# Performance work log

Hardware: AMD Instinct MI355X
Metric: run time of the kernel (lower is better)

The kernel has to match this reference:

```python
import jax, jax.numpy as jnp
import numpy as np

N, L = 5, 2097152
WIDTH = 11  # max_pool1d kernel width in the original


def setup_inputs() -> dict:
    key = jax.random.key(0)
    k1, k2 = jax.random.split(key)
    rppg = jax.random.normal(k1, (N, L), dtype=jnp.float32)
    ppg = jax.random.normal(k2, (N, L), dtype=jnp.float32)
    return {"rppg": rppg, "ppg": ppg, "fs": 30, "epoch": 15}


def _normalize(x):
    # normalize_torch: per-signal standardization
    mu = x.mean(axis=1, keepdims=True)
    sd = x.std(axis=1, keepdims=True)
    return (x - mu) / sd


def _window_max(x, width):
    # sliding max over centered window of `width`, same padding (-inf pad)
    return jax.lax.reduce_window(x, -jnp.inf, jax.lax.max,
                                 (1, width), (1, 1),
                                 [(0, 0), (width // 2, width // 2)])


def _mean_hr(x, fs):
    # A position p is a 'nice peak' iff max_pool argmax at p equals p,
    # i.e. x[p] is the max of its own centered window (ties have measure 0
    # for continuous signals). unique()+masking collapses to this mask.
    w = _window_max(x, WIDTH)
    m1 = x == w                                            # [N, L] peak mask
    npk = m1.sum(axis=1, keepdims=True).astype(x.dtype)
    mean_pk = (x * m1).sum(axis=1, keepdims=True) / npk    # mean of peak values
    m = m1 & (x > mean_pk / 2)                             # amplitude-filtered peaks
    idx = jnp.arange(x.shape[1])
    vals = jnp.where(m, idx, -1)
    # previous peak index strictly before p (fixed-shape replacement for diff
    # over a variable-length peak index list)
    prev = jnp.pad(jax.lax.cummax(vals, axis=1)[:, :-1], ((0, 0), (1, 0)),
                   constant_values=-1)
    valid = m & (prev >= 0)                                # one entry per inter-peak gap
    gaps = (idx[None, :] - prev).astype(x.dtype)
    inv = jnp.where(valid, 1.0 / gaps, 0.0)
    # mean(60 / (gap / fs)) = 60 * fs * mean(1 / gap)
    return (60.0 * fs) * inv.sum(axis=1) / valid.sum(axis=1).astype(x.dtype)


def reference(rppg, ppg, fs, epoch):
    ppg = _normalize(ppg.reshape(N, -1))
    rppg = _normalize(rppg.reshape(N, -1))
    ppg_hr = _mean_hr(ppg, fs)
    rppg_hr = _mean_hr(rppg, fs)
    # hr_score = mean_i |ppg_hr - rppg_hr| / ppg_hr  (peak_score is computed
    # in the original but not returned)
    return jnp.mean(jnp.abs(ppg_hr - rppg_hr) / ppg_hr)
```

## Files before the change

kernel.cpp:

```cpp
#include <hip/hip_runtime.h>
#include <math.h>
#include <limits.h>

namespace {

constexpr int LNUM = 2097152;
constexpr int NROW = 5;
constexpr int NSER = 10;
constexpr int TPB = 256;
constexpr int CHUNK = 4096;
constexpr int CPR = LNUM / CHUNK;
constexpr int NBLK = NSER * CPR;
constexpr int KIT = 4;

struct Agg { int first; int last; int c; double s; };

__device__ __forceinline__ Agg combine(const Agg& a, const Agg& b) {
  Agg r;
  r.first = (a.first >= 0) ? a.first : b.first;
  r.last  = (b.last >= 0) ? b.last : a.last;
  r.s = a.s + b.s;
  r.c = a.c + b.c;
  if (a.last >= 0 && b.first >= 0) {
    r.s += 1.0 / (double)(b.first - a.last);
    r.c += 1;
  }
  return r;
}

__device__ __forceinline__ const float* row_ptr(const float* rppg,
                                                const float* ppg, int rw) {
  return (rw < NROW) ? rppg + (size_t)rw * LNUM
                     : ppg + (size_t)(rw - NROW) * LNUM;
}

__device__ __forceinline__ void window4(const float* __restrict__ x, int p0,
                                        float X[4], float w[4]) {
  const float4 f = *reinterpret_cast<const float4*>(x + p0);
  X[0] = f.x; X[1] = f.y; X[2] = f.z; X[3] = f.w;
  float Y[14];
  Y[5] = X[0]; Y[6] = X[1]; Y[7] = X[2]; Y[8] = X[3];
  Y[1] = __shfl_up(X[0], 1);  Y[2] = __shfl_up(X[1], 1);
  Y[3] = __shfl_up(X[2], 1);  Y[4] = __shfl_up(X[3], 1);
  Y[0] = __shfl_up(X[3], 2);
  Y[9] = __shfl_down(X[0], 1);  Y[10] = __shfl_down(X[1], 1);
  Y[11] = __shfl_down(X[2], 1); Y[12] = __shfl_down(X[3], 1);
  Y[13] = __shfl_down(X[0], 2);
  const int lane = threadIdx.x & 63;
  if (lane == 0) {
#pragma unroll
    for (int j = 0; j < 5; ++j) {
      int g = p0 - 5 + j;
      Y[j] = (g >= 0) ? x[g] : -INFINITY;
    }
  } else if (lane == 1) {
    int g = p0 - 5;
    Y[0] = (g >= 0) ? x[g] : -INFINITY;
  }
  if (lane == 63) {
#pragma unroll
    for (int j = 0; j < 5; ++j) {
      int g = p0 + 4 + j;
      Y[9 + j] = (g < LNUM) ? x[g] : -INFINITY;
    }
  } else if (lane == 62) {
    int g = p0 + 8;
    Y[13] = (g < LNUM) ? x[g] : -INFINITY;
  }
  float m2[13];
#pragma unroll
  for (int i = 0; i < 13; ++i) m2[i] = fmaxf(Y[i], Y[i + 1]);
  float m4[11];
#pragma unroll
  for (int i = 0; i < 11; ++i) m4[i] = fmaxf(m2[i], m2[i + 2]);
  float m8[7];
#pragma unroll
  for (int i = 0; i < 7; ++i) m8[i] = fmaxf(m4[i], m4[i + 4]);
#pragma unroll
  for (int t = 0; t < 4; ++t) w[t] = fmaxf(m8[t], m8[t + 3]);
}

__global__ __launch_bounds__(TPB) void stats_kernel(
    const float* __restrict__ rppg, const float* __restrict__ ppg,
    double* __restrict__ psum, double* __restrict__ ppk,
    int* __restrict__ pnpk) {
  const int bid = blockIdx.x;
  const int rw = bid >> 9;
  const int chunk = bid & (CPR - 1);
  const float* x = row_ptr(rppg, ppg, rw);
  const int lane = threadIdx.x & 63;
  const int wid = threadIdx.x >> 6;
  const int segbase = chunk * CHUNK + wid * 1024;

  double tsum = 0.0, tpk = 0.0;
  int tn = 0;
  for (int k = 0; k < KIT; ++k) {
    const int p0 = segbase + k * 256 + 4 * lane;
    float X[4], w[4];
    window4(x, p0, X, w);
#pragma unroll
    for (int t = 0; t < 4; ++t) {
      tsum += (double)X[t];
      if (X[t] == w[t]) { tpk += (double)X[t]; ++tn; }
    }
  }
#pragma unroll
  for (int off = 32; off > 0; off >>= 1) {
    tsum += __shfl_down(tsum, off);
    tpk  += __shfl_down(tpk, off);
    tn   += __shfl_down(tn, off);
  }
  __shared__ double wsum[4], wpk[4];
  __shared__ int wn[4];
  if (lane == 0) { wsum[wid] = tsum; wpk[wid] = tpk; wn[wid] = tn; }
  __syncthreads();
  if (threadIdx.x == 0) {
    psum[bid] = wsum[0] + wsum[1] + wsum[2] + wsum[3];
    ppk[bid]  = wpk[0] + wpk[1] + wpk[2] + wpk[3];
    pnpk[bid] = wn[0] + wn[1] + wn[2] + wn[3];
  }
}

__global__ __launch_bounds__(TPB) void thresh_kernel(
    const double* __restrict__ psum, const double* __restrict__ ppk,
    const int* __restrict__ pnpk, double* __restrict__ thr) {
  const int r = blockIdx.x;
  const int t = threadIdx.x;
  const int lane = t & 63;
  const int wid = t >> 6;
  double s0 = psum[r * CPR + t] + psum[r * CPR + t + 256];
  double p0 = ppk[r * CPR + t] + ppk[r * CPR + t + 256];
  int n0 = pnpk[r * CPR + t] + pnpk[r * CPR + t + 256];
#pragma unroll
  for (int off = 32; off > 0; off >>= 1) {
    s0 += __shfl_down(s0, off);
    p0 += __shfl_down(p0, off);
    n0 += __shfl_down(n0, off);
  }
  __shared__ double ws[4], wp[4];
  __shared__ int wn[4];
  if (lane == 0) { ws[wid] = s0; wp[wid] = p0; wn[wid] = n0; }
  __syncthreads();
  if (t == 0) {
    double S = ws[0] + ws[1] + ws[2] + ws[3];
    double P = wp[0] + wp[1] + wp[2] + wp[3];
    double Nn = (double)(wn[0] + wn[1] + wn[2] + wn[3]);
    thr[r] = 0.5 * (S / (double)LNUM + P / Nn);
  }
}

__global__ __launch_bounds__(TPB) void gap_kernel(
    const float* __restrict__ rppg, const float* __restrict__ ppg,
    const double* __restrict__ thr,
    int* __restrict__ cfirst, int* __restrict__ clast,
    double* __restrict__ csum, int* __restrict__ ccnt) {
  const int bid = blockIdx.x;
  const int rw = bid >> 9;
  const int chunk = bid & (CPR - 1);
  const float* x = row_ptr(rppg, ppg, rw);
  const float th = (float)thr[rw];
  const int lane = threadIdx.x & 63;
  const int wid = threadIdx.x >> 6;
  const int segbase = chunk * CHUNK + wid * 1024;

  double lsum = 0.0;
  int lcnt = 0;
  int lfirst = INT_MAX;
  int carry = -1;
  for (int k = 0; k < KIT; ++k) {
    const int p0 = segbase + k * 256 + 4 * lane;
    float X[4], w[4];
    window4(x, p0, X, w);
    int pk = -1;
#pragma unroll
    for (int t = 0; t < 4; ++t)
      if (X[t] == w[t] && X[t] > th) pk = p0 + t;
    if (pk >= 0 && lfirst == INT_MAX) lfirst = pk;
    int m = pk;
#pragma unroll
    for (int off = 1; off < 64; off <<= 1) {
      int u = __shfl_up(m, off);
      if (lane >= off) m = max(m, u);
    }
    int excl = __shfl_up(m, 1);
    int prev = (lane == 0) ? carry : max(excl, carry);
    if (pk >= 0 && prev >= 0) {
      lsum += (double)(1.0f / (float)(pk - prev));
      ++lcnt;
    }
    int lastall = __shfl(m, 63);
    carry = max(carry, lastall);
  }
#pragma unroll
  for (int off = 32; off > 0; off >>= 1) {
    lsum += __shfl_down(lsum, off);
    lcnt += __shfl_down(lcnt, off);
    lfirst = min(lfirst, __shfl_down(lfirst, off));
  }
  __shared__ Agg waggs[4];
  if (lane == 0) {
    Agg a;
    a.first = (lfirst == INT_MAX) ? -1 : lfirst;
    a.last = carry;
    a.c = lcnt; a.s = lsum;
    waggs[wid] = a;
  }
  __syncthreads();
  if (threadIdx.x == 0) {
    Agg r = waggs[0];
    r = combine(r, waggs[1]);
    r = combine(r, waggs[2]);
    r = combine(r, waggs[3]);
    cfirst[bid] = r.first; clast[bid] = r.last;
    csum[bid] = r.s; ccnt[bid] = r.c;
  }
}

__global__ __launch_bounds__(TPB) void final_kernel(
    const int* __restrict__ cfirst, const int* __restrict__ clast,
    const double* __restrict__ csum, const int* __restrict__ ccnt,
    const int* __restrict__ fsp, float* __restrict__ out) {
  __shared__ Agg waggs[4];
  __shared__ double shr[NSER];
  const int t = threadIdx.x;
  const int lane = t & 63;
  const int wid = t >> 6;
  for (int r = 0; r < NSER; ++r) {
    const int i0 = r * CPR + 2 * t;
    Agg a0; a0.first = cfirst[i0];     a0.last = clast[i0];
    a0.c = ccnt[i0];                   a0.s = csum[i0];
    Agg a1; a1.first = cfirst[i0 + 1]; a1.last = clast[i0 + 1];
    a1.c = ccnt[i0 + 1];               a1.s = csum[i0 + 1];
    a0 = combine(a0, a1);
#pragma unroll
    for (int off = 1; off < 64; off <<= 1) {
      Agg b;
      b.first = __shfl_down(a0.first, off);
      b.last  = __shfl_down(a0.last, off);
      b.c     = __shfl_down(a0.c, off);
      b.s     = __shfl_down(a0.s, off);
      a0 = combine(a0, b);
    }
    if (lane == 0) waggs[wid] = a0;
    __syncthreads();
    if (t == 0) {
      Agg rr = waggs[0];
      rr = combine(rr, waggs[1]);
      rr = combine(rr, waggs[2]);
      rr = combine(rr, waggs[3]);
      shr[r] = 60.0 * (double)fsp[0] * rr.s / (double)rr.c;
    }
    __syncthreads();
  }
  if (t == 0) {
    double acc = 0.0;
    for (int r = 0; r < NROW; ++r)
      acc += fabs(shr[NROW + r] - shr[r]) / shr[NROW + r];
    out[0] = (float)(acc / (double)NROW);
  }
}

}

extern "C" void kernel_launch(void* const* d_in, const int* in_sizes, int n_in,
                              void* d_out, int out_size, void* d_ws, size_t ws_size,
                              hipStream_t stream) {
  const float* rppg = (const float*)d_in[0];
  const float* ppg  = (const float*)d_in[1];
  const int* fsp    = (const int*)d_in[2];
  float* out        = (float*)d_out;
  char* ws          = (char*)d_ws;

  double* psum   = (double*)(ws);
  double* ppk    = (double*)(ws + 40960);
  int*    pnpk   = (int*)(ws + 81920);
  double* csum   = (double*)(ws + 102400);
  int*    cfirst = (int*)(ws + 143360);
  int*    clast  = (int*)(ws + 163840);
  int*    ccnt   = (int*)(ws + 184320);
  double* thr    = (double*)(ws + 204800);

  stats_kernel<<<NBLK, TPB, 0, stream>>>(rppg, ppg, psum, ppk, pnpk);
  thresh_kernel<<<NSER, TPB, 0, stream>>>(psum, ppk, pnpk, thr);
  gap_kernel<<<NBLK, TPB, 0, stream>>>(rppg, ppg, thr, cfirst, clast, csum, ccnt);
  final_kernel<<<1, TPB, 0, stream>>>(cfirst, clast, csum, ccnt, fsp, out);
  (void)in_sizes; (void)n_in; (void)out_size; (void)ws_size;
}
```

Baseline: 170.7 us.

## Compact peak candidates in first pass so gap pass avoids rereading signals

The stats pass now writes each wavefront's local-max candidates (position and value) into compacted per-region slots using ballot and popcount. The gap pass reads only these compacted candidates and applies the threshold, instead of rereading the full 80 MB of input and recomputing window maxima. Final reduction now combines four times as many per-wavefront aggregates, and combine uses float reciprocal to match per-gap precision. Risk: the fixed slot size of 172 per 1024-element region assumes a bounded peak count, and extra scattered writes add traffic to the first pass.

```diff
diff --git a/kernel.cpp b/kernel.cpp
--- a/kernel.cpp
+++ b/kernel.cpp
@@ -12,6 +12,9 @@
 constexpr int CPR = LNUM / CHUNK;
 constexpr int NBLK = NSER * CPR;
 constexpr int KIT = 4;
+constexpr int SLOT = 172;
+constexpr int NREG = NBLK * 4;
+constexpr int RPR = NREG / NSER;
 
 struct Agg { int first; int last; int c; double s; };
 
@@ -22,7 +25,7 @@
   r.s = a.s + b.s;
   r.c = a.c + b.c;
   if (a.last >= 0 && b.first >= 0) {
-    r.s += 1.0 / (double)(b.first - a.last);
+    r.s += (double)(1.0f / (float)(b.first - a.last));
     r.c += 1;
   }
   return r;
@@ -83,7 +86,9 @@
 __global__ __launch_bounds__(TPB) void stats_kernel(
     const float* __restrict__ rppg, const float* __restrict__ ppg,
     double* __restrict__ psum, double* __restrict__ ppk,
-    int* __restrict__ pnpk) {
+    int* __restrict__ pnpk,
+    int* __restrict__ wpos, float* __restrict__ wval,
+    int* __restrict__ wcnt) {
   const int bid = blockIdx.x;
   const int rw = bid >> 9;
   const int chunk = bid & (CPR - 1);
@@ -91,19 +96,34 @@
   const int lane = threadIdx.x & 63;
   const int wid = threadIdx.x >> 6;
   const int segbase = chunk * CHUNK + wid * 1024;
+  const int region = bid * 4 + wid;
+  const int wbase = region * SLOT;
 
   double tsum = 0.0, tpk = 0.0;
   int tn = 0;
+  int wcount = 0;
   for (int k = 0; k < KIT; ++k) {
     const int p0 = segbase + k * 256 + 4 * lane;
     float X[4], w[4];
     window4(x, p0, X, w);
+    int off = -1;
+    float pv = 0.0f;
 #pragma unroll
     for (int t = 0; t < 4; ++t) {
       tsum += (double)X[t];
-      if (X[t] == w[t]) { tpk += (double)X[t]; ++tn; }
-    }
-  }
+      if (X[t] == w[t]) { tpk += (double)X[t]; ++tn; off = t; pv = X[t]; }
+    }
+    const bool cand = (off >= 0);
+    const unsigned long long bal = __ballot(cand);
+    const int rank = __popcll(bal & ((1ull << lane) - 1ull));
+    if (cand) {
+      wpos[wbase + wcount + rank] = p0 + off;
+      wval[wbase + wcount + rank] = pv;
+    }
+    wcount += __popcll(bal);
+  }
+  if (lane == 0) wcnt[region] = wcount;
+
 #pragma unroll
   for (int off = 32; off > 0; off >>= 1) {
     tsum += __shfl_down(tsum, off);
@@ -149,32 +169,30 @@
   }
 }
 
-__global__ __launch_bounds__(TPB) void gap_kernel(
-    const float* __restrict__ rppg, const float* __restrict__ ppg,
-    const double* __restrict__ thr,
-    int* __restrict__ cfirst, int* __restrict__ clast,
-    double* __restrict__ csum, int* __restrict__ ccnt) {
-  const int bid = blockIdx.x;
-  const int rw = bid >> 9;
-  const int chunk = bid & (CPR - 1);
-  const float* x = row_ptr(rppg, ppg, rw);
-  const float th = (float)thr[rw];
+__global__ __launch_bounds__(TPB) void gapc_kernel(
+    const int* __restrict__ wpos, const float* __restrict__ wval,
+    const int* __restrict__ wcnt, const double* __restrict__ thr,
+    int* __restrict__ afirst, int* __restrict__ alast,
+    double* __restrict__ asum, int* __restrict__ acnt) {
   const int lane = threadIdx.x & 63;
   const int wid = threadIdx.x >> 6;
-  const int segbase = chunk * CHUNK + wid * 1024;
+  const int region = blockIdx.x * 4 + wid;
+  const int rw = region / RPR;
+  const float th = (float)thr[rw];
+  const int cnt = wcnt[region];
+  const int base = region * SLOT;
 
   double lsum = 0.0;
   int lcnt = 0;
   int lfirst = INT_MAX;
   int carry = -1;
-  for (int k = 0; k < KIT; ++k) {
-    const int p0 = segbase + k * 256 + 4 * lane;
-    float X[4], w[4];
-    window4(x, p0, X, w);
+  for (int k = 0; k < 3; ++k) {
+    const int i = k * 64 + lane;
     int pk = -1;
-#pragma unroll
-    for (int t = 0; t < 4; ++t)
-      if (X[t] == w[t] && X[t] > th) pk = p0 + t;
+    if (i < cnt) {
+      float v = wval[base + i];
+      if (v > th) pk = wpos[base + i];
+    }
     if (pk >= 0 && lfirst == INT_MAX) lfirst = pk;
     int m = pk;
 #pragma unroll
@@ -197,28 +215,17 @@
     lcnt += __shfl_down(lcnt, off);
     lfirst = min(lfirst, __shfl_down(lfirst, off));
   }
-  __shared__ Agg waggs[4];
   if (lane == 0) {
-    Agg a;
-    a.first = (lfirst == INT_MAX) ? -1 : lfirst;
-    a.last = carry;
-    a.c = lcnt; a.s = lsum;
-    waggs[wid] = a;
-  }
-  __syncthreads();
-  if (threadIdx.x == 0) {
-    Agg r = waggs[0];
-    r = combine(r, waggs[1]);
-    r = combine(r, waggs[2]);
-    r = combine(r, waggs[3]);
-    cfirst[bid] = r.first; clast[bid] = r.last;
-    csum[bid] = r.s; ccnt[bid] = r.c;
+    afirst[region] = (lfirst == INT_MAX) ? -1 : lfirst;
+    alast[region] = carry;
+    acnt[region] = lcnt;
+    asum[region] = lsum;
   }
 }
 
 __global__ __launch_bounds__(TPB) void final_kernel(
-    const int* __restrict__ cfirst, const int* __restrict__ clast,
-    const double* __restrict__ csum, const int* __restrict__ ccnt,
+    const int* __restrict__ afirst, const int* __restrict__ alast,
+    const double* __restrict__ asum, const int* __restrict__ acnt,
     const int* __restrict__ fsp, float* __restrict__ out) {
   __shared__ Agg waggs[4];
   __shared__ double shr[NSER];
@@ -226,12 +233,15 @@
   const int lane = t & 63;
   const int wid = t >> 6;
   for (int r = 0; r < NSER; ++r) {
-    const int i0 = r * CPR + 2 * t;
-    Agg a0; a0.first = cfirst[i0];     a0.last = clast[i0];
-    a0.c = ccnt[i0];                   a0.s = csum[i0];
-    Agg a1; a1.first = cfirst[i0 + 1]; a1.last = clast[i0 + 1];
-    a1.c = ccnt[i0 + 1];               a1.s = csum[i0 + 1];
-    a0 = combine(a0, a1);
+    const int i0 = r * RPR + 8 * t;
+    Agg a0; a0.first = afirst[i0]; a0.last = alast[i0];
+    a0.c = acnt[i0];               a0.s = asum[i0];
+#pragma unroll
+    for (int j = 1; j < 8; ++j) {
+      Agg aj; aj.first = afirst[i0 + j]; aj.last = alast[i0 + j];
+      aj.c = acnt[i0 + j];               aj.s = asum[i0 + j];
+      a0 = combine(a0, aj);
+    }
 #pragma unroll
     for (int off = 1; off < 64; off <<= 1) {
       Agg b;
@@ -274,15 +284,20 @@
   double* psum   = (double*)(ws);
   double* ppk    = (double*)(ws + 40960);
   int*    pnpk   = (int*)(ws + 81920);
-  double* csum   = (double*)(ws + 102400);
-  int*    cfirst = (int*)(ws + 143360);
-  int*    clast  = (int*)(ws + 163840);
-  int*    ccnt   = (int*)(ws + 184320);
-  double* thr    = (double*)(ws + 204800);
-
-  stats_kernel<<<NBLK, TPB, 0, stream>>>(rppg, ppg, psum, ppk, pnpk);
+  double* thr    = (double*)(ws + 102400);
+  int*    afirst = (int*)(ws + 103424);
+  int*    alast  = (int*)(ws + 185344);
+  int*    acnt   = (int*)(ws + 267264);
+  double* asum   = (double*)(ws + 349184);
+  int*    wcnt   = (int*)(ws + 513024);
+  int*    wpos   = (int*)(ws + 594944);
+  float*  wval   = (float*)(ws + 14685184);
+
+  stats_kernel<<<NBLK, TPB, 0, stream>>>(rppg, ppg, psum, ppk, pnpk,
+                                         wpos, wval, wcnt);
   thresh_kernel<<<NSER, TPB, 0, stream>>>(psum, ppk, pnpk, thr);
-  gap_kernel<<<NBLK, TPB, 0, stream>>>(rppg, ppg, thr, cfirst, clast, csum, ccnt);
-  final_kernel<<<1, TPB, 0, stream>>>(cfirst, clast, csum, ccnt, fsp, out);
+  gapc_kernel<<<NBLK, TPB, 0, stream>>>(wpos, wval, wcnt, thr,
+                                        afirst, alast, asum, acnt);
+  final_kernel<<<1, TPB, 0, stream>>>(afirst, alast, asum, acnt, fsp, out);
   (void)in_sizes; (void)n_in; (void)out_size; (void)ws_size;
 }
```

New measurement: 184.0 us. 1.08x slower.
